# Optimization experiments

Measured on AMD Instinct MI355X. Metric: run time of the kernel, lower is better.

Reference implementation:

```python
import jax, jax.numpy as jnp
import numpy as np

V, E, H, S = 32000, 1024, 1024, 2048


def setup_inputs() -> dict:
    key = jax.random.key(0)
    ks = jax.random.split(key, 16)
    std = 0.02
    return {
        "encoder_out": jax.random.normal(ks[0], (S, E), jnp.float32),
        "word_input": jax.random.randint(ks[1], (1,), 0, V, jnp.int32),
        "last_context": jax.random.normal(ks[2], (1, H), jnp.float32),
        "h0": jnp.zeros((1, 1, H), jnp.float32),
        "c0": jnp.zeros((1, 1, H), jnp.float32),
        # learned parameters
        "emb": jax.random.normal(ks[3], (V, E), jnp.float32) * std,
        "W_ih": jax.random.normal(ks[4], (4 * H, E + H), jnp.float32) * std,
        "W_hh": jax.random.normal(ks[5], (4 * H, H), jnp.float32) * std,
        "b_ih": jnp.zeros((4 * H,), jnp.float32),
        "b_hh": jnp.zeros((4 * H,), jnp.float32),
        "W_attn": jax.random.normal(ks[6], (H, E + H), jnp.float32) * std,
        "b_attn": jnp.zeros((H,), jnp.float32),
        "v": jax.random.uniform(ks[7], (H,), jnp.float32) * 0.1,
        "W_ah": jax.random.normal(ks[8], (H, E + H), jnp.float32) * std,
        "b_ah": jnp.zeros((H,), jnp.float32),
        "W_out": jax.random.normal(ks[9], (V, H), jnp.float32) * std,
        "b_out": jnp.zeros((V,), jnp.float32),
    }


def reference(encoder_out, word_input, last_context, h0, c0,
              emb, W_ih, W_hh, b_ih, b_hh,
              W_attn, b_attn, v, W_ah, b_ah, W_out, b_out):
    # single decoder step, batch=1 (dropout in eval mode == identity)
    embedded = emb[word_input[0]]                       # [E]
    x = jnp.concatenate([last_context[0], embedded])    # [H+E] (context first, as in torch.cat)
    # LSTM cell (PyTorch gate order i, f, g, o)
    gates = W_ih @ x + b_ih + W_hh @ h0[0, 0] + b_hh    # [4H]
    i, f, g, o = jnp.split(gates, 4)
    c = jax.nn.sigmoid(f) * c0[0, 0] + jax.nn.sigmoid(i) * jnp.tanh(g)
    ht = jax.nn.sigmoid(o) * jnp.tanh(c)                # [H]
    # additive attention, vectorized over encoder steps.
    # original concatenates (ht, encoder_out[i]); split attn weight accordingly.
    Wa_h, Wa_e = W_attn[:, :H], W_attn[:, H:]
    scores = jnp.tanh(encoder_out @ Wa_e.T + (Wa_h @ ht + b_attn)) @ v  # [S]
    w = jax.nn.softmax(scores)                          # [S]
    context = w @ encoder_out                           # [E]
    ht_tilda = jnp.tanh(W_ah @ jnp.concatenate([context, ht]) + b_ah)  # [H]
    output = jax.nn.log_softmax(W_out @ ht_tilda + b_out)              # [V]
    return (output[None, :], (ht[None, None, :], c[None, None, :]),
            ht_tilda[None, :], w[None, :])
```

## Files before the change

kernel.cpp:

```cpp
#include <hip/hip_runtime.h>
#include <math.h>

#define V_ 32000
#define E_ 1024
#define H_ 1024
#define S_ 2048

typedef __attribute__((ext_vector_type(8))) short bf16x8;
typedef __attribute__((ext_vector_type(8))) unsigned short u16x8;
typedef __attribute__((ext_vector_type(4))) float f32x4;

typedef __attribute__((address_space(1))) const unsigned int gu32;
typedef __attribute__((address_space(3))) unsigned int lu32;

__device__ __forceinline__ float sigmoidf_(float x) { return 1.0f / (1.0f + expf(-x)); }

__device__ __forceinline__ unsigned short f2bf(float f) {
    unsigned int u = __builtin_bit_cast(unsigned int, f);
    unsigned int r = (u + 0x7fffu + ((u >> 16) & 1u)) >> 16;
    return (unsigned short)r;
}

__device__ __forceinline__ u16x8 pack8(float4 a, float4 b) {
    u16x8 p;
    p[0] = f2bf(a.x); p[1] = f2bf(a.y); p[2] = f2bf(a.z); p[3] = f2bf(a.w);
    p[4] = f2bf(b.x); p[5] = f2bf(b.y); p[6] = f2bf(b.z); p[7] = f2bf(b.w);
    return p;
}

__device__ __forceinline__ void gload16(const void* g, void* l) {
    __builtin_amdgcn_global_load_lds((gu32*)g, (lu32*)l, 16, 0, 0);
}

__global__ __launch_bounds__(256) void k1_gates(
    const float* __restrict__ W_ih, const float* __restrict__ W_hh,
    const float* __restrict__ b_ih, const float* __restrict__ b_hh,
    const float* __restrict__ last_context, const float* __restrict__ emb,
    const int* __restrict__ word, const float* __restrict__ h0,
    const float* __restrict__ c0,
    float* __restrict__ out_ht, float* __restrict__ out_c,
    float* __restrict__ ws_ht)
{
    __shared__ float sbuf[4];
    int j = blockIdx.x;
    int tid = threadIdx.x, wave = tid >> 6, lane = tid & 63;
    const float* embrow = emb + (size_t)word[0] * E_;
    int row = j + wave * H_;
    const float* wi = W_ih + (size_t)row * (E_ + H_);
    const float* wh = W_hh + (size_t)row * H_;
    float acc = 0.f;
    #pragma unroll
    for (int it = 0; it < 8; ++it) {
        int idx = (lane + it * 64) * 4;
        float4 wv = *(const float4*)(wi + idx);
        float4 xv = (idx < H_) ? *(const float4*)(last_context + idx)
                               : *(const float4*)(embrow + (idx - H_));
        acc = fmaf(wv.x, xv.x, acc); acc = fmaf(wv.y, xv.y, acc);
        acc = fmaf(wv.z, xv.z, acc); acc = fmaf(wv.w, xv.w, acc);
    }
    #pragma unroll
    for (int it = 0; it < 4; ++it) {
        int idx = (lane + it * 64) * 4;
        float4 wv = *(const float4*)(wh + idx);
        float4 hv = *(const float4*)(h0 + idx);
        acc = fmaf(wv.x, hv.x, acc); acc = fmaf(wv.y, hv.y, acc);
        acc = fmaf(wv.z, hv.z, acc); acc = fmaf(wv.w, hv.w, acc);
    }
    #pragma unroll
    for (int m = 32; m; m >>= 1) acc += __shfl_down(acc, m, 64);
    if (lane == 0) sbuf[wave] = acc;
    __syncthreads();
    if (tid == 0) {
        float gi = sbuf[0] + b_ih[j]          + b_hh[j];
        float gf = sbuf[1] + b_ih[j + H_]     + b_hh[j + H_];
        float gg = sbuf[2] + b_ih[j + 2*H_]   + b_hh[j + 2*H_];
        float go = sbuf[3] + b_ih[j + 3*H_]   + b_hh[j + 3*H_];
        float c  = sigmoidf_(gf) * c0[j] + sigmoidf_(gi) * tanhf(gg);
        float ht = sigmoidf_(go) * tanhf(c);
        out_c[j]  = c;
        out_ht[j] = ht;
        ws_ht[j]  = ht;
    }
}

__global__ __launch_bounds__(64) void k2_q(
    const float* __restrict__ W_attn, const float* __restrict__ b_attn,
    const float* __restrict__ ht, float* __restrict__ q)
{
    int h = blockIdx.x;
    int lane = threadIdx.x;
    const float* row = W_attn + (size_t)h * (E_ + H_);
    float acc = 0.f;
    #pragma unroll
    for (int it = 0; it < 4; ++it) {
        int idx = (lane + it * 64) * 4;
        float4 wv = *(const float4*)(row + idx);
        float4 hv = *(const float4*)(ht + idx);
        acc = fmaf(wv.x, hv.x, acc); acc = fmaf(wv.y, hv.y, acc);
        acc = fmaf(wv.z, hv.z, acc); acc = fmaf(wv.w, hv.w, acc);
    }
    #pragma unroll
    for (int m = 32; m; m >>= 1) acc += __shfl_down(acc, m, 64);
    if (lane == 0) q[h] = acc + b_attn[h];
}

__global__ __launch_bounds__(256) void k3a_conv(
    const float* __restrict__ enc, const float* __restrict__ W_attn,
    unsigned short* __restrict__ encb, unsigned short* __restrict__ wab)
{
    int idx = blockIdx.x * 256 + threadIdx.x;
    const int ENC_CH = (S_ * E_) / 8;
    const float* src;
    unsigned short* dst;
    if (idx < ENC_CH) {
        src = enc + (size_t)idx * 8;
        dst = encb + (size_t)idx * 8;
    } else {
        int w = idx - ENC_CH;
        int h = w >> 7, off = (w & 127) * 8;
        src = W_attn + (size_t)h * (E_ + H_) + H_ + off;
        dst = wab + (size_t)h * E_ + off;
    }
    float4 a = *(const float4*)src;
    float4 b = *(const float4*)(src + 4);
    *(u16x8*)dst = pack8(a, b);
}

__global__ __launch_bounds__(256) void k3b_gemm(
    const unsigned short* __restrict__ encb, const unsigned short* __restrict__ wab,
    const float* __restrict__ q, const float* __restrict__ v,
    float* __restrict__ spart)
{
    __shared__ unsigned short As[2][128 * 64];
    __shared__ unsigned short Bs[2][64 * 64];
    int s0 = blockIdx.x * 128, h0 = blockIdx.y * 64;
    int tid = threadIdx.x;
    int wave = tid >> 6, lane = tid & 63;
    int wr = (wave >> 1) * 64, wc = (wave & 1) * 32;

    int srow = tid >> 3;
    int lch  = ((tid & 7) ^ (srow & 7)) * 8;
    const unsigned short* aSrc[4];
    #pragma unroll
    for (int jj = 0; jj < 4; ++jj)
        aSrc[jj] = encb + (size_t)(s0 + jj * 32 + srow) * E_ + lch;
    const unsigned short* bSrc[2];
    #pragma unroll
    for (int jj = 0; jj < 2; ++jj)
        bSrc[jj] = wab + (size_t)(h0 + jj * 32 + srow) * E_ + lch;

    int fc = lane & 15, g = lane >> 4;
    int aRow[4], bRow[2], pc[2];
    #pragma unroll
    for (int m = 0; m < 4; ++m) aRow[m] = (wr + m * 16 + fc) * 64;
    #pragma unroll
    for (int n = 0; n < 2; ++n) bRow[n] = (wc + n * 16 + fc) * 64;
    #pragma unroll
    for (int kk = 0; kk < 2; ++kk) pc[kk] = ((kk * 4 + g) ^ (fc & 7)) * 8;

    f32x4 acc[4][2];
    #pragma unroll
    for (int m = 0; m < 4; ++m)
        #pragma unroll
        for (int n = 0; n < 2; ++n)
            acc[m][n] = (f32x4){0.f, 0.f, 0.f, 0.f};

    #pragma unroll
    for (int jj = 0; jj < 4; ++jj) gload16(aSrc[jj], &As[0][jj * 2048 + tid * 8]);
    #pragma unroll
    for (int jj = 0; jj < 2; ++jj) gload16(bSrc[jj], &Bs[0][jj * 2048 + tid * 8]);
    __syncthreads();

    int cur = 0;
    for (int t = 0; t < 16; ++t) {
        if (t < 15) {
            int k0 = (t + 1) * 64;
            #pragma unroll
            for (int jj = 0; jj < 4; ++jj)
                gload16(aSrc[jj] + k0, &As[cur ^ 1][jj * 2048 + tid * 8]);
            #pragma unroll
            for (int jj = 0; jj < 2; ++jj)
                gload16(bSrc[jj] + k0, &Bs[cur ^ 1][jj * 2048 + tid * 8]);
        }
        #pragma unroll
        for (int kk = 0; kk < 2; ++kk) {
            bf16x8 af[4], bf2[2];
            #pragma unroll
            for (int m = 0; m < 4; ++m) af[m] = *(const bf16x8*)&As[cur][aRow[m] + pc[kk]];
            #pragma unroll
            for (int n = 0; n < 2; ++n) bf2[n] = *(const bf16x8*)&Bs[cur][bRow[n] + pc[kk]];
            #pragma unroll
            for (int m = 0; m < 4; ++m)
                #pragma unroll
                for (int n = 0; n < 2; ++n)
                    acc[m][n] = __builtin_amdgcn_mfma_f32_16x16x32_bf16(
                        af[m], bf2[n], acc[m][n], 0, 0, 0);
        }
        __syncthreads();
        cur ^= 1;
    }

    float qv[2], vv[2];
    #pragma unroll
    for (int n = 0; n < 2; ++n) {
        int col = h0 + wc + n * 16 + fc;
        qv[n] = q[col];
        vv[n] = v[col];
    }
    int part = blockIdx.y * 2 + (wave & 1);
    #pragma unroll
    for (int m = 0; m < 4; ++m) {
        #pragma unroll
        for (int j = 0; j < 4; ++j) {
            float p = 0.f;
            #pragma unroll
            for (int n = 0; n < 2; ++n)
                p += tanhf(acc[m][n][j] + qv[n]) * vv[n];
            #pragma unroll
            for (int mask = 8; mask; mask >>= 1) p += __shfl_xor(p, mask, 64);
            if (fc == 0)
                spart[(size_t)(s0 + wr + m * 16 + g * 4 + j) * 32 + part] = p;
        }
    }
}

__global__ __launch_bounds__(256) void k4_softmax(
    const float* __restrict__ spart, float* __restrict__ w_out,
    float* __restrict__ w_ws, float* __restrict__ ctx)
{
    __shared__ float sm[4];
    int tid = threadIdx.x;
    #pragma unroll
    for (int i = 0; i < 4; ++i) ctx[tid + i * 256] = 0.f;
    float x[8];
    float m = -1e30f;
    #pragma unroll
    for (int i = 0; i < 8; ++i) {
        int e = tid + i * 256;
        float acc = 0.f;
        #pragma unroll
        for (int c = 0; c < 8; ++c) {
            float4 pv = *(const float4*)&spart[(size_t)e * 32 + c * 4];
            acc += pv.x + pv.y + pv.z + pv.w;
        }
        x[i] = acc;
        m = fmaxf(m, acc);
    }
    #pragma unroll
    for (int s = 32; s; s >>= 1) m = fmaxf(m, __shfl_xor(m, s, 64));
    if ((tid & 63) == 0) sm[tid >> 6] = m;
    __syncthreads();
    m = fmaxf(fmaxf(sm[0], sm[1]), fmaxf(sm[2], sm[3]));
    float sum = 0.f;
    #pragma unroll
    for (int i = 0; i < 8; ++i) { x[i] = expf(x[i] - m); sum += x[i]; }
    #pragma unroll
    for (int s = 32; s; s >>= 1) sum += __shfl_xor(sum, s, 64);
    __syncthreads();
    if ((tid & 63) == 0) sm[tid >> 6] = sum;
    __syncthreads();
    sum = sm[0] + sm[1] + sm[2] + sm[3];
    float inv = 1.0f / sum;
    #pragma unroll
    for (int i = 0; i < 8; ++i) {
        float wv = x[i] * inv;
        w_out[tid + i * 256] = wv;
        w_ws[tid + i * 256]  = wv;
    }
}

__global__ __launch_bounds__(256) void k5_context(
    const float* __restrict__ enc, const float* __restrict__ w,
    float* __restrict__ context)
{
    int e = blockIdx.x * 256 + threadIdx.x;
    int s_begin = blockIdx.y * 64;
    float acc = 0.f;
    #pragma unroll 4
    for (int s = s_begin; s < s_begin + 64; ++s)
        acc = fmaf(w[s], enc[(size_t)s * E_ + e], acc);
    atomicAdd(&context[e], acc);
}

__global__ __launch_bounds__(64) void k6_htilda(
    const float* __restrict__ W_ah, const float* __restrict__ b_ah,
    const float* __restrict__ context, const float* __restrict__ ht,
    float* __restrict__ out_htt, float* __restrict__ ws_htt)
{
    int h = blockIdx.x;
    int lane = threadIdx.x;
    const float* row = W_ah + (size_t)h * (E_ + H_);
    float acc = 0.f;
    #pragma unroll
    for (int it = 0; it < 8; ++it) {
        int idx = (lane + it * 64) * 4;
        float4 wv = *(const float4*)(row + idx);
        float4 xv = (idx < E_) ? *(const float4*)(context + idx)
                               : *(const float4*)(ht + idx - E_);
        acc = fmaf(wv.x, xv.x, acc); acc = fmaf(wv.y, xv.y, acc);
        acc = fmaf(wv.z, xv.z, acc); acc = fmaf(wv.w, xv.w, acc);
    }
    #pragma unroll
    for (int m = 32; m; m >>= 1) acc += __shfl_down(acc, m, 64);
    if (lane == 0) {
        float val = tanhf(acc + b_ah[h]);
        out_htt[h] = val;
        ws_htt[h]  = val;
    }
}

__global__ __launch_bounds__(256) void k7_logits(
    const float* __restrict__ W_out, const float* __restrict__ b_out,
    const float* __restrict__ ht_tilda, float* __restrict__ logits)
{
    int row = blockIdx.x * 4 + (threadIdx.x >> 6);
    int lane = threadIdx.x & 63;
    const float* wr = W_out + (size_t)row * H_;
    float acc = 0.f;
    #pragma unroll
    for (int it = 0; it < 4; ++it) {
        int idx = (lane + it * 64) * 4;
        float4 wv = *(const float4*)(wr + idx);
        float4 hv = *(const float4*)(ht_tilda + idx);
        acc = fmaf(wv.x, hv.x, acc); acc = fmaf(wv.y, hv.y, acc);
        acc = fmaf(wv.z, hv.z, acc); acc = fmaf(wv.w, hv.w, acc);
    }
    #pragma unroll
    for (int m = 32; m; m >>= 1) acc += __shfl_down(acc, m, 64);
    if (lane == 0) logits[row] = acc + b_out[row];
}

__global__ __launch_bounds__(256) void k8_partial(
    const float* __restrict__ logits, float* __restrict__ part)
{
    __shared__ float smx[4], ssx[4];
    int b = blockIdx.x, tid = threadIdx.x;
    int base = b * 500;
    float m = -1e30f, s = 0.f;
    for (int i = tid; i < 500; i += 256) {
        float x = logits[base + i];
        float M = fmaxf(m, x);
        s = s * expf(m - M) + expf(x - M);
        m = M;
    }
    #pragma unroll
    for (int mask = 32; mask; mask >>= 1) {
        float om = __shfl_xor(m, mask, 64);
        float os = __shfl_xor(s, mask, 64);
        float M = fmaxf(m, om);
        s = s * expf(m - M) + os * expf(om - M);
        m = M;
    }
    if ((tid & 63) == 0) { smx[tid >> 6] = m; ssx[tid >> 6] = s; }
    __syncthreads();
    if (tid == 0) {
        float M = fmaxf(fmaxf(smx[0], smx[1]), fmaxf(smx[2], smx[3]));
        float S = ssx[0] * expf(smx[0] - M) + ssx[1] * expf(smx[1] - M)
                + ssx[2] * expf(smx[2] - M) + ssx[3] * expf(smx[3] - M);
        part[2 * b]     = M;
        part[2 * b + 1] = S;
    }
}

__global__ __launch_bounds__(256) void k9_finish(
    float* __restrict__ out, const float* __restrict__ part)
{
    __shared__ float slse;
    int tid = threadIdx.x;
    if (tid < 64) {
        float m = part[2 * tid], s = part[2 * tid + 1];
        #pragma unroll
        for (int mask = 32; mask; mask >>= 1) {
            float om = __shfl_xor(m, mask, 64);
            float os = __shfl_xor(s, mask, 64);
            float M = fmaxf(m, om);
            s = s * expf(m - M) + os * expf(om - M);
            m = M;
        }
        if (tid == 0) slse = m + logf(s);
    }
    __syncthreads();
    out[blockIdx.x * 256 + tid] -= slse;
}

extern "C" void kernel_launch(void* const* d_in, const int* in_sizes, int n_in,
                              void* d_out, int out_size, void* d_ws, size_t ws_size,
                              hipStream_t stream) {
    const float* enc          = (const float*)d_in[0];
    const int*   word         = (const int*)  d_in[1];
    const float* last_context = (const float*)d_in[2];
    const float* h0           = (const float*)d_in[3];
    const float* c0           = (const float*)d_in[4];
    const float* emb          = (const float*)d_in[5];
    const float* W_ih         = (const float*)d_in[6];
    const float* W_hh         = (const float*)d_in[7];
    const float* b_ih         = (const float*)d_in[8];
    const float* b_hh         = (const float*)d_in[9];
    const float* W_attn       = (const float*)d_in[10];
    const float* b_attn       = (const float*)d_in[11];
    const float* v            = (const float*)d_in[12];
    const float* W_ah         = (const float*)d_in[13];
    const float* b_ah         = (const float*)d_in[14];
    const float* W_out        = (const float*)d_in[15];
    const float* b_out        = (const float*)d_in[16];

    float* out        = (float*)d_out;
    float* out_logits = out;
    float* out_ht     = out + V_;
    float* out_c      = out + V_ + H_;
    float* out_htt    = out + V_ + 2 * H_;
    float* out_w      = out + V_ + 3 * H_;

    float* ws        = (float*)d_ws;
    float* ws_ht     = ws;
    float* ws_q      = ws + 1024;
    float* ws_w      = ws + 2048;
    float* ws_ctx    = ws + 4096;
    float* ws_htt    = ws + 5120;
    float* ws_part   = ws + 6144;
    float* ws_spart  = ws + 8192;
    unsigned short* encb = (unsigned short*)(ws + 73728);
    unsigned short* wab  = encb + (size_t)S_ * E_;

    k1_gates<<<1024, 256, 0, stream>>>(W_ih, W_hh, b_ih, b_hh, last_context, emb,
                                       word, h0, c0, out_ht, out_c, ws_ht);
    k2_q<<<1024, 64, 0, stream>>>(W_attn, b_attn, ws_ht, ws_q);
    k3a_conv<<<1536, 256, 0, stream>>>(enc, W_attn, encb, wab);
    k3b_gemm<<<dim3(S_ / 128, H_ / 64), 256, 0, stream>>>(encb, wab, ws_q, v, ws_spart);
    k4_softmax<<<1, 256, 0, stream>>>(ws_spart, out_w, ws_w, ws_ctx);
    k5_context<<<dim3(4, 32), 256, 0, stream>>>(enc, ws_w, ws_ctx);
    k6_htilda<<<1024, 64, 0, stream>>>(W_ah, b_ah, ws_ctx, ws_ht, out_htt, ws_htt);
    k7_logits<<<8000, 256, 0, stream>>>(W_out, b_out, ws_htt, out_logits);
    k8_partial<<<64, 256, 0, stream>>>(out_logits, ws_part);
    k9_finish<<<125, 256, 0, stream>>>(out_logits, ws_part);
}
```

Measured before the change: 91.90 us.

## Fuse kernels, drop softmax max-subtraction, compute context from bf16 encoder

Merges the LSTM gate kernel with the bf16 conversion pass into one launch. Replaces the single-block attention softmax plus context kernel with a 128-block kernel that computes unnormalized exp weights and partial context from bf16 encoder rows, deferring normalization to the h-tilda kernel, which also writes the weights. The logits log-softmax drops max-subtraction and the partial kernel, accumulating exp sums in the logits kernel. This cuts launches and serial single-block stages, but removes max-stabilization, so large scores or logits could overflow, and lowers context precision to bf16.

After: 92.11 us. No clear change (+0.2%).

```diff
diff --git a/kernel.cpp b/kernel.cpp
--- a/kernel.cpp
+++ b/kernel.cpp
@@ -20,70 +20,105 @@
     unsigned int r = (u + 0x7fffu + ((u >> 16) & 1u)) >> 16;
     return (unsigned short)r;
 }
-
+__device__ __forceinline__ float bf2f(unsigned short u) {
+    return __builtin_bit_cast(float, ((unsigned int)u) << 16);
+}
 __device__ __forceinline__ u16x8 pack8(float4 a, float4 b) {
     u16x8 p;
     p[0] = f2bf(a.x); p[1] = f2bf(a.y); p[2] = f2bf(a.z); p[3] = f2bf(a.w);
     p[4] = f2bf(b.x); p[5] = f2bf(b.y); p[6] = f2bf(b.z); p[7] = f2bf(b.w);
     return p;
 }
-
 __device__ __forceinline__ void gload16(const void* g, void* l) {
     __builtin_amdgcn_global_load_lds((gu32*)g, (lu32*)l, 16, 0, 0);
 }
 
-__global__ __launch_bounds__(256) void k1_gates(
+__global__ __launch_bounds__(256) void kA(
     const float* __restrict__ W_ih, const float* __restrict__ W_hh,
     const float* __restrict__ b_ih, const float* __restrict__ b_hh,
     const float* __restrict__ last_context, const float* __restrict__ emb,
     const int* __restrict__ word, const float* __restrict__ h0,
-    const float* __restrict__ c0,
+    const float* __restrict__ c0, const float* __restrict__ enc,
+    const float* __restrict__ W_attn,
     float* __restrict__ out_ht, float* __restrict__ out_c,
-    float* __restrict__ ws_ht)
-{
-    __shared__ float sbuf[4];
-    int j = blockIdx.x;
-    int tid = threadIdx.x, wave = tid >> 6, lane = tid & 63;
-    const float* embrow = emb + (size_t)word[0] * E_;
-    int row = j + wave * H_;
-    const float* wi = W_ih + (size_t)row * (E_ + H_);
-    const float* wh = W_hh + (size_t)row * H_;
-    float acc = 0.f;
-    #pragma unroll
-    for (int it = 0; it < 8; ++it) {
-        int idx = (lane + it * 64) * 4;
-        float4 wv = *(const float4*)(wi + idx);
-        float4 xv = (idx < H_) ? *(const float4*)(last_context + idx)
-                               : *(const float4*)(embrow + (idx - H_));
-        acc = fmaf(wv.x, xv.x, acc); acc = fmaf(wv.y, xv.y, acc);
-        acc = fmaf(wv.z, xv.z, acc); acc = fmaf(wv.w, xv.w, acc);
-    }
-    #pragma unroll
-    for (int it = 0; it < 4; ++it) {
-        int idx = (lane + it * 64) * 4;
-        float4 wv = *(const float4*)(wh + idx);
-        float4 hv = *(const float4*)(h0 + idx);
-        acc = fmaf(wv.x, hv.x, acc); acc = fmaf(wv.y, hv.y, acc);
-        acc = fmaf(wv.z, hv.z, acc); acc = fmaf(wv.w, hv.w, acc);
-    }
-    #pragma unroll
-    for (int m = 32; m; m >>= 1) acc += __shfl_down(acc, m, 64);
-    if (lane == 0) sbuf[wave] = acc;
-    __syncthreads();
-    if (tid == 0) {
-        float gi = sbuf[0] + b_ih[j]          + b_hh[j];
-        float gf = sbuf[1] + b_ih[j + H_]     + b_hh[j + H_];
-        float gg = sbuf[2] + b_ih[j + 2*H_]   + b_hh[j + 2*H_];
-        float go = sbuf[3] + b_ih[j + 3*H_]   + b_hh[j + 3*H_];
-        float c  = sigmoidf_(gf) * c0[j] + sigmoidf_(gi) * tanhf(gg);
-        float ht = sigmoidf_(go) * tanhf(c);
-        out_c[j]  = c;
-        out_ht[j] = ht;
-        ws_ht[j]  = ht;
-    }
-}
-
-__global__ __launch_bounds__(64) void k2_q(
+    float* __restrict__ ws_ht, unsigned short* __restrict__ encb,
+    unsigned short* __restrict__ wab, float* __restrict__ ws_ctx)
+{
+    int b = blockIdx.x, tid = threadIdx.x;
+    int wave = tid >> 6, lane = tid & 63;
+    if (b < 1024) {
+        __shared__ float sbuf[4];
+        int j = b;
+        const float* embrow = emb + (size_t)word[0] * E_;
+        int row = j + wave * H_;
+        const float* wi = W_ih + (size_t)row * (E_ + H_);
+        const float* wh = W_hh + (size_t)row * H_;
+        float acc = 0.f;
+        #pragma unroll
+        for (int it = 0; it < 8; ++it) {
+            int idx = (lane + it * 64) * 4;
+            float4 wv = *(const float4*)(wi + idx);
+            float4 xv = (idx < H_) ? *(const float4*)(last_context + idx)
+                                   : *(const float4*)(embrow + (idx - H_));
+            acc = fmaf(wv.x, xv.x, acc); acc = fmaf(wv.y, xv.y, acc);
+            acc = fmaf(wv.z, xv.z, acc); acc = fmaf(wv.w, xv.w, acc);
+        }
+        #pragma unroll
+        for (int it = 0; it < 4; ++it) {
+            int idx = (lane + it * 64) * 4;
+            float4 wv = *(const float4*)(wh + idx);
+            float4 hv = *(const float4*)(h0 + idx);
+            acc = fmaf(wv.x, hv.x, acc); acc = fmaf(wv.y, hv.y, acc);
+            acc = fmaf(wv.z, hv.z, acc); acc = fmaf(wv.w, hv.w, acc);
+        }
+        #pragma unroll
+        for (int m = 32; m; m >>= 1) acc += __shfl_down(acc, m, 64);
+        if (lane == 0) sbuf[wave] = acc;
+        __syncthreads();
+        if (tid < 4 && b == 0) {
+        }
+        if (tid == 0) {
+            float gi = sbuf[0] + b_ih[j]          + b_hh[j];
+            float gf = sbuf[1] + b_ih[j + H_]     + b_hh[j + H_];
+            float gg = sbuf[2] + b_ih[j + 2*H_]   + b_hh[j + 2*H_];
+            float go = sbuf[3] + b_ih[j + 3*H_]   + b_hh[j + 3*H_];
+            float c  = sigmoidf_(gf) * c0[j] + sigmoidf_(gi) * tanhf(gg);
+            float ht = sigmoidf_(go) * tanhf(c);
+            out_c[j]  = c;
+            out_ht[j] = ht;
+            ws_ht[j]  = ht;
+        }
+        if (b == 0) {
+            ws_ctx[tid] = 0.f;
+            ws_ctx[tid + 256] = 0.f;
+            ws_ctx[tid + 512] = 0.f;
+            ws_ctx[tid + 768] = 0.f;
+        }
+    } else {
+        int cid = (b - 1024) * 256 + tid;
+        const int ENC_CH = (S_ * E_) / 8;
+        #pragma unroll
+        for (int i = 0; i < 3; ++i) {
+            int idx = cid + i * 131072;
+            const float* src;
+            unsigned short* dst;
+            if (idx < ENC_CH) {
+                src = enc + (size_t)idx * 8;
+                dst = encb + (size_t)idx * 8;
+            } else {
+                int w = idx - ENC_CH;
+                int h = w >> 7, off = (w & 127) * 8;
+                src = W_attn + (size_t)h * (E_ + H_) + H_ + off;
+                dst = wab + (size_t)h * E_ + off;
+            }
+            float4 a = *(const float4*)src;
+            float4 bq = *(const float4*)(src + 4);
+            *(u16x8*)dst = pack8(a, bq);
+        }
+    }
+}
+
+__global__ __launch_bounds__(64) void kB(
     const float* __restrict__ W_attn, const float* __restrict__ b_attn,
     const float* __restrict__ ht, float* __restrict__ q)
 {
@@ -104,29 +139,7 @@
     if (lane == 0) q[h] = acc + b_attn[h];
 }
 
-__global__ __launch_bounds__(256) void k3a_conv(
-    const float* __restrict__ enc, const float* __restrict__ W_attn,
-    unsigned short* __restrict__ encb, unsigned short* __restrict__ wab)
-{
-    int idx = blockIdx.x * 256 + threadIdx.x;
-    const int ENC_CH = (S_ * E_) / 8;
-    const float* src;
-    unsigned short* dst;
-    if (idx < ENC_CH) {
-        src = enc + (size_t)idx * 8;
-        dst = encb + (size_t)idx * 8;
-    } else {
-        int w = idx - ENC_CH;
-        int h = w >> 7, off = (w & 127) * 8;
-        src = W_attn + (size_t)h * (E_ + H_) + H_ + off;
-        dst = wab + (size_t)h * E_ + off;
-    }
-    float4 a = *(const float4*)src;
-    float4 b = *(const float4*)(src + 4);
-    *(u16x8*)dst = pack8(a, b);
-}
-
-__global__ __launch_bounds__(256) void k3b_gemm(
+__global__ __launch_bounds__(256) void kC(
     const unsigned short* __restrict__ encb, const unsigned short* __restrict__ wab,
     const float* __restrict__ q, const float* __restrict__ v,
     float* __restrict__ spart)
@@ -224,97 +237,102 @@
     }
 }
 
-__global__ __launch_bounds__(256) void k4_softmax(
-    const float* __restrict__ spart, float* __restrict__ w_out,
-    float* __restrict__ w_ws, float* __restrict__ ctx)
-{
-    __shared__ float sm[4];
-    int tid = threadIdx.x;
-    #pragma unroll
-    for (int i = 0; i < 4; ++i) ctx[tid + i * 256] = 0.f;
-    float x[8];
-    float m = -1e30f;
-    #pragma unroll
-    for (int i = 0; i < 8; ++i) {
-        int e = tid + i * 256;
-        float acc = 0.f;
-        #pragma unroll
-        for (int c = 0; c < 8; ++c) {
-            float4 pv = *(const float4*)&spart[(size_t)e * 32 + c * 4];
-            acc += pv.x + pv.y + pv.z + pv.w;
-        }
-        x[i] = acc;
-        m = fmaxf(m, acc);
-    }
-    #pragma unroll
-    for (int s = 32; s; s >>= 1) m = fmaxf(m, __shfl_xor(m, s, 64));
-    if ((tid & 63) == 0) sm[tid >> 6] = m;
+__global__ __launch_bounds__(256) void kD(
+    const float* __restrict__ spart, const unsigned short* __restrict__ encb,
+    float* __restrict__ expw, float* __restrict__ gpart, float* __restrict__ ctx)
+{
+    __shared__ float esh[16];
+    int b = blockIdx.x, tid = threadIdx.x;
+    int s0 = b * 16;
+    int sl = tid >> 4, pp = tid & 15;
+    float vsum = spart[(size_t)(s0 + sl) * 32 + pp]
+               + spart[(size_t)(s0 + sl) * 32 + pp + 16];
+    #pragma unroll
+    for (int mask = 8; mask; mask >>= 1) vsum += __shfl_xor(vsum, mask, 64);
+    if (pp == 0) {
+        float e = expf(vsum);
+        expw[s0 + sl] = e;
+        esh[sl] = e;
+    }
     __syncthreads();
-    m = fmaxf(fmaxf(sm[0], sm[1]), fmaxf(sm[2], sm[3]));
-    float sum = 0.f;
-    #pragma unroll
-    for (int i = 0; i < 8; ++i) { x[i] = expf(x[i] - m); sum += x[i]; }
-    #pragma unroll
-    for (int s = 32; s; s >>= 1) sum += __shfl_xor(sum, s, 64);
-    __syncthreads();
-    if ((tid & 63) == 0) sm[tid >> 6] = sum;
-    __syncthreads();
-    sum = sm[0] + sm[1] + sm[2] + sm[3];
-    float inv = 1.0f / sum;
-    #pragma unroll
-    for (int i = 0; i < 8; ++i) {
-        float wv = x[i] * inv;
-        w_out[tid + i * 256] = wv;
-        w_ws[tid + i * 256]  = wv;
-    }
-}
-
-__global__ __launch_bounds__(256) void k5_context(
-    const float* __restrict__ enc, const float* __restrict__ w,
-    float* __restrict__ context)
-{
-    int e = blockIdx.x * 256 + threadIdx.x;
-    int s_begin = blockIdx.y * 64;
-    float acc = 0.f;
-    #pragma unroll 4
-    for (int s = s_begin; s < s_begin + 64; ++s)
-        acc = fmaf(w[s], enc[(size_t)s * E_ + e], acc);
-    atomicAdd(&context[e], acc);
-}
-
-__global__ __launch_bounds__(64) void k6_htilda(
+    if (tid == 0) {
+        float bs = 0.f;
+        #pragma unroll
+        for (int i = 0; i < 16; ++i) bs += esh[i];
+        gpart[b] = bs;
+    }
+    int e0 = tid * 4;
+    float a0 = 0.f, a1 = 0.f, a2 = 0.f, a3 = 0.f;
+    #pragma unroll
+    for (int ss = 0; ss < 16; ++ss) {
+        const unsigned short* r = encb + (size_t)(s0 + ss) * E_ + e0;
+        ushort4 u = *(const ushort4*)r;
+        float w = esh[ss];
+        a0 = fmaf(w, bf2f(u.x), a0);
+        a1 = fmaf(w, bf2f(u.y), a1);
+        a2 = fmaf(w, bf2f(u.z), a2);
+        a3 = fmaf(w, bf2f(u.w), a3);
+    }
+    atomicAdd(&ctx[e0 + 0], a0);
+    atomicAdd(&ctx[e0 + 1], a1);
+    atomicAdd(&ctx[e0 + 2], a2);
+    atomicAdd(&ctx[e0 + 3], a3);
+}
+
+__global__ __launch_bounds__(64) void kE(
     const float* __restrict__ W_ah, const float* __restrict__ b_ah,
-    const float* __restrict__ context, const float* __restrict__ ht,
-    float* __restrict__ out_htt, float* __restrict__ ws_htt)
-{
-    int h = blockIdx.x;
+    const float* __restrict__ ctx, const float* __restrict__ ht,
+    const float* __restrict__ gpart, const float* __restrict__ expw,
+    float* __restrict__ out_htt, float* __restrict__ ws_htt,
+    float* __restrict__ out_w)
+{
+    int b = blockIdx.x;
     int lane = threadIdx.x;
-    const float* row = W_ah + (size_t)h * (E_ + H_);
+    float gsum = gpart[lane] + gpart[lane + 64];
+    #pragma unroll
+    for (int m = 32; m; m >>= 1) gsum += __shfl_xor(gsum, m, 64);
+    float invS = 1.0f / gsum;
+    if (b >= 1024) {
+        int s = (b - 1024) * 256 + lane * 4;
+        float4 e4 = *(const float4*)(expw + s);
+        float4 w4 = { e4.x * invS, e4.y * invS, e4.z * invS, e4.w * invS };
+        *(float4*)(out_w + s) = w4;
+        return;
+    }
+    const float* row = W_ah + (size_t)b * (E_ + H_);
     float acc = 0.f;
     #pragma unroll
     for (int it = 0; it < 8; ++it) {
         int idx = (lane + it * 64) * 4;
         float4 wv = *(const float4*)(row + idx);
-        float4 xv = (idx < E_) ? *(const float4*)(context + idx)
-                               : *(const float4*)(ht + idx - E_);
+        float4 xv;
+        if (idx < E_) {
+            float4 cv = *(const float4*)(ctx + idx);
+            xv = (float4){ cv.x * invS, cv.y * invS, cv.z * invS, cv.w * invS };
+        } else {
+            xv = *(const float4*)(ht + idx - E_);
+        }
         acc = fmaf(wv.x, xv.x, acc); acc = fmaf(wv.y, xv.y, acc);
         acc = fmaf(wv.z, xv.z, acc); acc = fmaf(wv.w, xv.w, acc);
     }
     #pragma unroll
     for (int m = 32; m; m >>= 1) acc += __shfl_down(acc, m, 64);
     if (lane == 0) {
-        float val = tanhf(acc + b_ah[h]);
-        out_htt[h] = val;
-        ws_htt[h]  = val;
-    }
-}
-
-__global__ __launch_bounds__(256) void k7_logits(
+        float val = tanhf(acc + b_ah[b]);
+        out_htt[b] = val;
+        ws_htt[b]  = val;
+    }
+}
+
+__global__ __launch_bounds__(256) void kF(
     const float* __restrict__ W_out, const float* __restrict__ b_out,
-    const float* __restrict__ ht_tilda, float* __restrict__ logits)
-{
-    int row = blockIdx.x * 4 + (threadIdx.x >> 6);
-    int lane = threadIdx.x & 63;
+    const float* __restrict__ ht_tilda, float* __restrict__ logits,
+    float* __restrict__ lpart)
+{
+    __shared__ float wes[4];
+    int b = blockIdx.x;
+    int wave = threadIdx.x >> 6, lane = threadIdx.x & 63;
+    int row = b * 4 + wave;
     const float* wr = W_out + (size_t)row * H_;
     float acc = 0.f;
     #pragma unroll
@@ -327,60 +345,29 @@
     }
     #pragma unroll
     for (int m = 32; m; m >>= 1) acc += __shfl_down(acc, m, 64);
-    if (lane == 0) logits[row] = acc + b_out[row];
-}
-
-__global__ __launch_bounds__(256) void k8_partial(
-    const float* __restrict__ logits, float* __restrict__ part)
-{
-    __shared__ float smx[4], ssx[4];
-    int b = blockIdx.x, tid = threadIdx.x;
-    int base = b * 500;
-    float m = -1e30f, s = 0.f;
-    for (int i = tid; i < 500; i += 256) {
-        float x = logits[base + i];
-        float M = fmaxf(m, x);
-        s = s * expf(m - M) + expf(x - M);
-        m = M;
-    }
-    #pragma unroll
-    for (int mask = 32; mask; mask >>= 1) {
-        float om = __shfl_xor(m, mask, 64);
-        float os = __shfl_xor(s, mask, 64);
-        float M = fmaxf(m, om);
-        s = s * expf(m - M) + os * expf(om - M);
-        m = M;
-    }
-    if ((tid & 63) == 0) { smx[tid >> 6] = m; ssx[tid >> 6] = s; }
+    if (lane == 0) {
+        float lg = acc + b_out[row];
+        logits[row] = lg;
+        wes[wave] = expf(lg);
+    }
     __syncthreads();
-    if (tid == 0) {
-        float M = fmaxf(fmaxf(smx[0], smx[1]), fmaxf(smx[2], smx[3]));
-        float S = ssx[0] * expf(smx[0] - M) + ssx[1] * expf(smx[1] - M)
-                + ssx[2] * expf(smx[2] - M) + ssx[3] * expf(smx[3] - M);
-        part[2 * b]     = M;
-        part[2 * b + 1] = S;
-    }
-}
-
-__global__ __launch_bounds__(256) void k9_finish(
-    float* __restrict__ out, const float* __restrict__ part)
-{
-    __shared__ float slse;
+    if (threadIdx.x == 0)
+        lpart[b] = wes[0] + wes[1] + wes[2] + wes[3];
+}
+
+__global__ __launch_bounds__(256) void kG(
+    float* __restrict__ out, const float* __restrict__ lpart)
+{
+    __shared__ float sred[4];
     int tid = threadIdx.x;
-    if (tid < 64) {
-        float m = part[2 * tid], s = part[2 * tid + 1];
-        #pragma unroll
-        for (int mask = 32; mask; mask >>= 1) {
-            float om = __shfl_xor(m, mask, 64);
-            float os = __shfl_xor(s, mask, 64);
-            float M = fmaxf(m, om);
-            s = s * expf(m - M) + os * expf(om - M);
-            m = M;
-        }
-        if (tid == 0) slse = m + logf(s);
-    }
+    float s = 0.f;
+    for (int i = tid; i < 8000; i += 256) s += lpart[i];
+    #pragma unroll
+    for (int m = 32; m; m >>= 1) s += __shfl_down(s, m, 64);
+    if ((tid & 63) == 0) sred[tid >> 6] = s;
     __syncthreads();
-    out[blockIdx.x * 256 + tid] -= slse;
+    float lse = logf(sred[0] + sred[1] + sred[2] + sred[3]);
+    out[blockIdx.x * 256 + tid] -= lse;
 }
 
 extern "C" void kernel_launch(void* const* d_in, const int* in_sizes, int n_in,
@@ -411,26 +398,26 @@
     float* out_htt    = out + V_ + 2 * H_;
     float* out_w      = out + V_ + 3 * H_;
 
-    float* ws        = (float*)d_ws;
-    float* ws_ht     = ws;
-    float* ws_q      = ws + 1024;
-    float* ws_w      = ws + 2048;
-    float* ws_ctx    = ws + 4096;
-    float* ws_htt    = ws + 5120;
-    float* ws_part   = ws + 6144;
-    float* ws_spart  = ws + 8192;
-    unsigned short* encb = (unsigned short*)(ws + 73728);
+    float* ws      = (float*)d_ws;
+    float* ws_ht   = ws;
+    float* ws_q    = ws + 1024;
+    float* ws_expw = ws + 2048;
+    float* ws_ctx  = ws + 4096;
+    float* ws_htt  = ws + 5120;
+    float* ws_gp   = ws + 6144;
+    float* ws_lp   = ws + 8192;
+    float* ws_sp   = ws + 16384;
+    unsigned short* encb = (unsigned short*)(ws + 81920);
     unsigned short* wab  = encb + (size_t)S_ * E_;
 
-    k1_gates<<<1024, 256, 0, stream>>>(W_ih, W_hh, b_ih, b_hh, last_context, emb,
-                                       word, h0, c0, out_ht, out_c, ws_ht);
-    k2_q<<<1024, 64, 0, stream>>>(W_attn, b_attn, ws_ht, ws_q);
-    k3a_conv<<<1536, 256, 0, stream>>>(enc, W_attn, encb, wab);
-    k3b_gemm<<<dim3(S_ / 128, H_ / 64), 256, 0, stream>>>(encb, wab, ws_q, v, ws_spart);
-    k4_softmax<<<1, 256, 0, stream>>>(ws_spart, out_w, ws_w, ws_ctx);
-    k5_context<<<dim3(4, 32), 256, 0, stream>>>(enc, ws_w, ws_ctx);
-    k6_htilda<<<1024, 64, 0, stream>>>(W_ah, b_ah, ws_ctx, ws_ht, out_htt, ws_htt);
-    k7_logits<<<8000, 256, 0, stream>>>(W_out, b_out, ws_htt, out_logits);
-    k8_partial<<<64, 256, 0, stream>>>(out_logits, ws_part);
-    k9_finish<<<125, 256, 0, stream>>>(out_logits, ws_part);
-}
+    kA<<<1536, 256, 0, stream>>>(W_ih, W_hh, b_ih, b_hh, last_context, emb, word,
+                                 h0, c0, enc, W_attn, out_ht, out_c, ws_ht,
+                                 encb, wab, ws_ctx);
+    kB<<<1024, 64, 0, stream>>>(W_attn, b_attn, ws_ht, ws_q);
+    kC<<<dim3(S_ / 128, H_ / 64), 256, 0, stream>>>(encb, wab, ws_q, v, ws_sp);
+    kD<<<128, 256, 0, stream>>>(ws_sp, encb, ws_expw, ws_gp, ws_ctx);
+    kE<<<1032, 64, 0, stream>>>(W_ah, b_ah, ws_ctx, ws_ht, ws_gp, ws_expw,
+                                out_htt, ws_htt, out_w);
+    kF<<<8000, 256, 0, stream>>>(W_out, b_out, ws_htt, out_logits, ws_lp);
+    kG<<<125, 256, 0, stream>>>(out_logits, ws_lp);
+}
```
